# Kernel optimization log

Hardware: AMD Instinct MI355X
Metric: run time of the kernel (lower is better)

## Reference

```python
import jax, jax.numpy as jnp
import numpy as np
import itertools


def exclude_mask(n, d):
    # Boolean mask over d object axes of size n: True iff all indices pairwise distinct.
    if d <= 1:
        return jnp.ones((n,) * d, dtype=bool)
    idx = [jnp.arange(n).reshape((1,) * i + (n,) + (1,) * (d - 1 - i)) for i in range(d)]
    m = jnp.ones((n,) * d, dtype=bool)
    for i in range(d):
        for j in range(i + 1, d):
            m = m & (idx[i] != idx[j])
    return m


def reduce_group(x, d, exclude_self=True):
    # x: [B, n^d (d object axes), C] -> [B, n^(d-1), 2C]
    # exists = max over last object axis (masked to 0), forall = min (masked to 1),
    # interleaved per channel as in torch.stack(..., dim=-1).view(..., 2C).
    if exclude_self and d > 1:
        n = x.shape[1]
        m = exclude_mask(n, d)[None, ..., None]
        x0 = jnp.where(m, x, 0.0)
        x1 = jnp.where(m, x, 1.0)
    else:
        x0 = x1 = x
    ex = jnp.max(x0, axis=-2)
    fa = jnp.min(x1, axis=-2)
    out = jnp.stack([ex, fa], axis=-1)  # [..., C, 2]
    return out.reshape(out.shape[:-2] + (out.shape[-2] * 2,))


def expand_group(x, n):
    # Insert a new object axis of size n just before the channel axis (broadcast).
    return jnp.broadcast_to(jnp.expand_dims(x, -2), x.shape[:-1] + (n, x.shape[-1]))


def permute_group(x, d):
    # Concatenate all d! permutations of the last d object axes along channels.
    if d <= 1:
        return x
    nd = x.ndim
    obj_axes = list(range(nd - 1 - d, nd - 1))
    res = []
    for perm in itertools.permutations(obj_axes):
        p = list(range(0, nd - 1 - d)) + list(perm) + [nd - 1]
        res.append(jnp.transpose(x, p))
    return jnp.concatenate(res, axis=-1)


def mlp(x, W1, b1, W2, b2):
    # InferenceLayer: Linear -> ReLU -> Linear -> Sigmoid, applied on channel dim.
    h = jax.nn.relu(x @ W1 + b1)
    return jax.nn.sigmoid(h @ W2 + b2)


def setup_inputs() -> dict:
    key = jax.random.key(0)
    ks = jax.random.split(key, 24)
    B, n, C, H = 4, 48, 16, 64
    cin = {0: 48, 1: 64, 2: 128, 3: 192}
    inp = {
        "x0": jax.random.uniform(ks[0], (B, C), dtype=jnp.float32),
        "x1": jax.random.uniform(ks[1], (B, n, C), dtype=jnp.float32),
        "x2": jax.random.uniform(ks[2], (B, n, n, C), dtype=jnp.float32),
        "x3": jax.random.uniform(ks[3], (B, n, n, n, C), dtype=jnp.float32),
    }
    for g in range(4):
        inp[f"W1_{g}"] = 0.05 * jax.random.normal(ks[4 + 4 * g], (cin[g], H), dtype=jnp.float32)
        inp[f"b1_{g}"] = jnp.zeros((H,), dtype=jnp.float32)
        inp[f"W2_{g}"] = 0.05 * jax.random.normal(ks[5 + 4 * g], (H, C), dtype=jnp.float32)
        inp[f"b2_{g}"] = jnp.zeros((C,), dtype=jnp.float32)
    return inp


def reference(x0, x1, x2, x3,
              W1_0, b1_0, W2_0, b2_0,
              W1_1, b1_1, W2_1, b2_1,
              W1_2, b1_2, W2_2, b2_2,
              W1_3, b1_3, W2_3, b2_3):
    n = x1.shape[1]
    # group 0: [self, reduce(group1)] -> MLP
    t0 = jnp.concatenate([x0, reduce_group(x1, 1)], axis=-1)            # [B, 48]
    o0 = mlp(t0, W1_0, b1_0, W2_0, b2_0)
    # group 1: [expand(group0), self, reduce(group2)] -> MLP (permuter d=1 is identity)
    t1 = jnp.concatenate([expand_group(x0, n), x1, reduce_group(x2, 2)], axis=-1)  # [B,n,64]
    o1 = mlp(t1, W1_1, b1_1, W2_1, b2_1)
    # group 2: [expand(group1), self, reduce(group3)] -> permute(d=2) -> MLP
    t2 = jnp.concatenate([expand_group(x1, n), x2, reduce_group(x3, 3)], axis=-1)  # [B,n,n,64]
    t2 = permute_group(t2, 2)                                           # [B,n,n,128]
    o2 = mlp(t2, W1_2, b1_2, W2_2, b2_2)
    # group 3: [expand(group2), self] -> permute(d=3) -> MLP
    t3 = jnp.concatenate([expand_group(x2, n), x3], axis=-1)            # [B,n,n,n,32]
    t3 = permute_group(t3, 3)                                           # [B,n,n,n,192]
    o3 = mlp(t3, W1_3, b1_3, W2_3, b2_3)
    return (o0, o1, o2, o3)
```

## Files before the change

### kernel.cpp

```cpp
#include <hip/hip_runtime.h>
#include <math.h>

#define NN 48

typedef __attribute__((ext_vector_type(8))) short bf16x8;
typedef __attribute__((ext_vector_type(4))) float f32x4;

__device__ __forceinline__ float sigmoidf_(float x) {
    return 1.0f / (1.0f + __expf(-x));
}

__device__ __forceinline__ unsigned short f2bf(float f) {
    unsigned u = __float_as_uint(f);
    return (unsigned short)((u + 0x7fffu + ((u >> 16) & 1u)) >> 16);
}

__device__ __forceinline__ unsigned packbf2(float a, float b) {
    return (unsigned)f2bf(a) | ((unsigned)f2bf(b) << 16);
}

__global__ __launch_bounds__(256) void k_pre(const float* __restrict__ x2, const float* __restrict__ x3,
        const float* __restrict__ W1, const float* __restrict__ W2,
        float* __restrict__ r3, unsigned short* __restrict__ wf,
        unsigned short* __restrict__ x2bf, unsigned short* __restrict__ x3bf, int emit) {
    int tid = threadIdx.x, blk = blockIdx.x;
    if (blk < 2304) {
        int posl = tid >> 6, l = tid & 63;
        int pos = blk * 4 + posl;
        int j = pos % NN, i = (pos / NN) % NN;
        int cq = l & 3, kkb = l >> 2;
        float4 ex = make_float4(0.f, 0.f, 0.f, 0.f);
        float4 fa = make_float4(1.f, 1.f, 1.f, 1.f);
        #pragma unroll
        for (int s = 0; s < 3; ++s) {
            int kk = kkb + s * 16;
            size_t idx = (((size_t)pos * NN + kk) << 4) + (cq << 2);
            float4 v = *(const float4*)(x3 + idx);
            if (emit) {
                uint2 pk;
                pk.x = packbf2(v.x, v.y);
                pk.y = packbf2(v.z, v.w);
                *(uint2*)(x3bf + idx) = pk;
            }
            bool ok = (i != j) && (kk != i) && (kk != j);
            ex.x = fmaxf(ex.x, ok ? v.x : 0.f);  fa.x = fminf(fa.x, ok ? v.x : 1.f);
            ex.y = fmaxf(ex.y, ok ? v.y : 0.f);  fa.y = fminf(fa.y, ok ? v.y : 1.f);
            ex.z = fmaxf(ex.z, ok ? v.z : 0.f);  fa.z = fminf(fa.z, ok ? v.z : 1.f);
            ex.w = fmaxf(ex.w, ok ? v.w : 0.f);  fa.w = fminf(fa.w, ok ? v.w : 1.f);
        }
        #pragma unroll
        for (int m = 4; m <= 32; m <<= 1) {
            ex.x = fmaxf(ex.x, __shfl_xor(ex.x, m));  fa.x = fminf(fa.x, __shfl_xor(fa.x, m));
            ex.y = fmaxf(ex.y, __shfl_xor(ex.y, m));  fa.y = fminf(fa.y, __shfl_xor(fa.y, m));
            ex.z = fmaxf(ex.z, __shfl_xor(ex.z, m));  fa.z = fminf(fa.z, __shfl_xor(fa.z, m));
            ex.w = fmaxf(ex.w, __shfl_xor(ex.w, m));  fa.w = fminf(fa.w, __shfl_xor(fa.w, m));
        }
        if (kkb == 0) {
            float* dst = r3 + ((size_t)pos << 5) + (cq << 3);
            *(float4*)dst       = make_float4(ex.x, fa.x, ex.y, fa.y);
            *(float4*)(dst + 4) = make_float4(ex.z, fa.z, ex.w, fa.w);
        }
    } else if (blk < 2340) {
        if (!emit) return;
        int bb = blk - 2304;
        #pragma unroll
        for (int q = 0; q < 4; ++q) {
            int e = bb * 1024 + q * 256 + tid;
            int off = e << 2;
            float4 v = *(const float4*)(x2 + off);
            uint2 pk;
            pk.x = packbf2(v.x, v.y);
            pk.y = packbf2(v.z, v.w);
            *(uint2*)(x2bf + off) = pk;
        }
    } else {
        for (int e = tid; e < 13312; e += 256) {
            unsigned short v;
            if (e < 12288) {
                int idx = e & 7, l = (e >> 3) & 63, r = e >> 9;
                int ks = r % 6, nt = r / 6;
                v = f2bf(W1[(ks * 32 + ((l >> 4) << 3) + idx) * 64 + (nt << 4) + (l & 15)]);
            } else {
                int e2 = e - 12288;
                int idx = e2 & 7, l = (e2 >> 3) & 63, ks = e2 >> 9;
                v = f2bf(W2[(ks * 32 + ((l >> 4) << 3) + idx) * 16 + (l & 15)]);
            }
            wf[e] = v;
        }
    }
}

__global__ __launch_bounds__(256) void k_small(const float* __restrict__ x0, const float* __restrict__ x1,
        const float* __restrict__ x2, const float* __restrict__ r3,
        const float* __restrict__ W1_0, const float* __restrict__ b1_0,
        const float* __restrict__ W2_0, const float* __restrict__ b2_0,
        const float* __restrict__ W1_1, const float* __restrict__ b1_1,
        const float* __restrict__ W2_1, const float* __restrict__ b2_1,
        const float* __restrict__ W1_2, const float* __restrict__ b1_2,
        const float* __restrict__ W2_2, const float* __restrict__ b2_2,
        float* __restrict__ out) {
    __shared__ __align__(16) float smem[8960];
    int tid = threadIdx.x;
    int blk = blockIdx.x;
    if (blk == 0) {
        float* st0 = smem;
        float* sh0 = smem + 192;
        int b = tid >> 6, sub = (tid >> 4) & 3, c = tid & 15;
        float ex = -INFINITY, fa = INFINITY;
        for (int ii = sub * 12; ii < sub * 12 + 12; ++ii) {
            float v = x1[(b * NN + ii) * 16 + c];
            ex = fmaxf(ex, v); fa = fminf(fa, v);
        }
        ex = fmaxf(ex, __shfl_xor(ex, 16)); fa = fminf(fa, __shfl_xor(fa, 16));
        ex = fmaxf(ex, __shfl_xor(ex, 32)); fa = fminf(fa, __shfl_xor(fa, 32));
        if (sub == 0) { st0[b * 48 + 16 + 2 * c] = ex; st0[b * 48 + 17 + 2 * c] = fa; }
        if (tid < 64) st0[(tid >> 4) * 48 + (tid & 15)] = x0[tid];
        __syncthreads();
        {
            int bb = tid >> 6, ln = tid & 63;
            float h = b1_0[ln];
            for (int cc = 0; cc < 48; ++cc) h += st0[bb * 48 + cc] * W1_0[cc * 64 + ln];
            sh0[bb * 64 + ln] = fmaxf(h, 0.f);
        }
        __syncthreads();
        if (tid < 64) {
            int bb = tid >> 4, o = tid & 15;
            float acc = b2_0[o];
            for (int tt = 0; tt < 64; ++tt) acc += sh0[bb * 64 + tt] * W2_0[tt * 16 + o];
            out[bb * 16 + o] = sigmoidf_(acc);
        }
    } else if (blk <= 48) {
        int grp = tid >> 6, ln = tid & 63;
        int row = (blk - 1) * 4 + grp;
        int b = row / NN, i = row % NN;
        float* sin1 = smem + grp * 64;
        float* sh1  = smem + 256 + grp * 64;
        int c = ln & 15, q = ln >> 4;
        float ex = 0.f, fa = 1.f;
        const float* xb = x2 + (size_t)row * NN * 16 + c;
        for (int jj = q * 12; jj < q * 12 + 12; ++jj) {
            float v = xb[jj * 16];
            bool ok = (jj != i);
            ex = fmaxf(ex, ok ? v : 0.f); fa = fminf(fa, ok ? v : 1.f);
        }
        ex = fmaxf(ex, __shfl_xor(ex, 16)); fa = fminf(fa, __shfl_xor(fa, 16));
        ex = fmaxf(ex, __shfl_xor(ex, 32)); fa = fminf(fa, __shfl_xor(fa, 32));
        if (q == 0) { sin1[32 + 2 * c] = ex; sin1[33 + 2 * c] = fa; }
        if (ln < 16) sin1[ln] = x0[b * 16 + ln];
        else if (ln < 32) sin1[ln] = x1[row * 16 + (ln - 16)];
        __syncthreads();
        float h = b1_1[ln];
        #pragma unroll
        for (int c4 = 0; c4 < 64; c4 += 4) {
            float4 iv = *(const float4*)&sin1[c4];
            h += iv.x * W1_1[(c4 + 0) * 64 + ln] + iv.y * W1_1[(c4 + 1) * 64 + ln]
               + iv.z * W1_1[(c4 + 2) * 64 + ln] + iv.w * W1_1[(c4 + 3) * 64 + ln];
        }
        sh1[ln] = fmaxf(h, 0.f);
        __syncthreads();
        if (ln < 16) {
            float acc = b2_1[ln];
            #pragma unroll
            for (int tt = 0; tt < 64; ++tt) acc += sh1[tt] * W2_1[tt * 16 + ln];
            out[64 + row * 16 + ln] = sigmoidf_(acc);
        }
    } else {
        float* sW1  = smem;
        float* sin_ = smem + 8192;
        float* sh   = smem + 8704;
        int wv = tid >> 6, ln = tid & 63;
        for (int p = tid; p < 8192; p += 256) sW1[p] = W1_2[p];
        float bias = b1_2[ln];
        __syncthreads();
        for (int rr = 0; rr < 4; ++rr) {
            int row = (blk - 49) * 16 + rr * 4 + wv;
            int j = row % NN;
            int bi = row / NN;
            int i = bi % NN;
            int b = bi / NN;
            for (int cc = ln; cc < 128; cc += 64) {
                int half = cc >> 6, w = cc & 63;
                int a1 = half ? j : i;
                int a2 = half ? i : j;
                float v;
                if (w < 16)      v = x1[(b * NN + a1) * 16 + w];
                else if (w < 32) v = x2[((b * NN + a1) * NN + a2) * 16 + (w - 16)];
                else             v = r3[((size_t)(b * NN + a1) * NN + a2) * 32 + (w - 32)];
                sin_[wv * 128 + cc] = v;
            }
            __syncthreads();
            float h = bias;
            #pragma unroll
            for (int c4 = 0; c4 < 128; c4 += 4) {
                float4 iv = *(const float4*)&sin_[wv * 128 + c4];
                h += iv.x * sW1[(c4 + 0) * 64 + ln] + iv.y * sW1[(c4 + 1) * 64 + ln]
                   + iv.z * sW1[(c4 + 2) * 64 + ln] + iv.w * sW1[(c4 + 3) * 64 + ln];
            }
            sh[wv * 64 + ln] = fmaxf(h, 0.f);
            __syncthreads();
            if (ln < 16) {
                float acc = b2_2[ln];
                #pragma unroll
                for (int tt = 0; tt < 64; ++tt) acc += sh[wv * 64 + tt] * W2_2[tt * 16 + ln];
                out[3136 + row * 16 + ln] = sigmoidf_(acc);
            }
            __syncthreads();
        }
    }
}

__global__ __launch_bounds__(192) void k_g3d(const unsigned short* __restrict__ x2bf,
        const unsigned short* __restrict__ x3bf, const unsigned short* __restrict__ wf,
        const float* __restrict__ b1, const float* __restrict__ b2,
        float* __restrict__ out3) {
    __shared__ __align__(16) unsigned short sH[2][6 * 64 * 8];

    int tid = threadIdx.x, mt = tid >> 6, l = tid & 63;
    int pp = blockIdx.x, i = 0;
    while (pp >= NN - i) { pp -= NN - i; ++i; }
    int j = i + pp;
    int b = blockIdx.y;

    bf16x8 w1f[4][6];
    #pragma unroll
    for (int nt = 0; nt < 4; ++nt)
        #pragma unroll
        for (int ks = 0; ks < 6; ++ks)
            w1f[nt][ks] = *(const bf16x8*)(wf + (((nt * 6 + ks) << 6) + l) * 8);
    bf16x8 w2f[2];
    #pragma unroll
    for (int ks = 0; ks < 2; ++ks)
        w2f[ks] = *(const bf16x8*)(wf + 12288 + ((ks << 6) + l) * 8);

    const int b2b = b * 36864;
    const int b3b = b * 1769472;
    const int cb2_[6] = { b2b + (i * NN + j) * 16, b2b + i * 768, b2b + (j * NN + i) * 16,
                          b2b + i * 16,            b2b + j * 768, b2b + j * 16 };
    const int cb3_[6] = { b3b + (i * NN + j) * 768, b3b + i * 36864 + j * 16, b3b + (j * NN + i) * 768,
                          b3b + i * 768 + j * 16,   b3b + j * 36864 + i * 16, b3b + j * 768 + i * 16 };
    const int s2_[6] = { 0, 16, 0, 768, 16, 768 };
    const int s3_[6] = { 16, 768, 16, 36864, 768, 36864 };

    int l15 = l & 15, g = l >> 4;
    bool isx2 = (g < 2);
    int goff = (g & 1) << 3;
    const unsigned short* bp = isx2 ? x2bf : x3bf;
    int off_[6];
    #pragma unroll
    for (int f = 0; f < 6; ++f) {
        int s = isx2 ? s2_[f] : s3_[f];
        int base = isx2 ? cb2_[f] : cb3_[f];
        off_[f] = base + ((mt << 4) + l15) * s + goff;
    }

    f32x4 acc[4][2];
    #pragma unroll
    for (int nt = 0; nt < 4; ++nt) {
        float bv = b1[(nt << 4) + l15];
        f32x4 t = {bv, bv, bv, bv};
        acc[nt][0] = t; acc[nt][1] = t;
    }
    const int p1[6] = { 2, 4, 0, 5, 1, 3 };

    #pragma unroll
    for (int f = 0; f < 6; ++f) {
        bf16x8 a = *(const bf16x8*)(bp + off_[f]);
        #pragma unroll
        for (int nt = 0; nt < 4; ++nt) {
            acc[nt][0] = __builtin_amdgcn_mfma_f32_16x16x32_bf16(a, w1f[nt][f], acc[nt][0], 0, 0, 0);
            acc[nt][1] = __builtin_amdgcn_mfma_f32_16x16x32_bf16(a, w1f[nt][p1[f]], acc[nt][1], 0, 0, 0);
        }
    }

    {
        int rbase = (l >> 4) << 2;
        #pragma unroll
        for (int tr = 0; tr < 2; ++tr) {
            #pragma unroll
            for (int nt = 0; nt < 4; ++nt) {
                int within = ((nt & 1) << 4) + l15;
                int ks2 = nt >> 1;
                int lhi = (within >> 3) << 4;
                int idx = within & 7;
                #pragma unroll
                for (int rg = 0; rg < 4; ++rg) {
                    float h = fmaxf(acc[nt][tr][rg], 0.0f);
                    int lp = rbase + rg + lhi;
                    sH[tr][((((mt << 1) + ks2) << 6) + lp) * 8 + idx] = f2bf(h);
                }
            }
        }
    }
    __syncthreads();

    {
        float bv2 = b2[l15];
        #pragma unroll
        for (int tr = 0; tr < 2; ++tr) {
            if (tr == 0 || i != j) {
                f32x4 acc2 = {bv2, bv2, bv2, bv2};
                #pragma unroll
                for (int ks = 0; ks < 2; ++ks) {
                    bf16x8 a = *(const bf16x8*)&sH[tr][((((mt << 1) + ks) << 6) + l) << 3];
                    acc2 = __builtin_amdgcn_mfma_f32_16x16x32_bf16(a, w2f[ks], acc2, 0, 0, 0);
                }
                int triple = tr ? ((b * NN + j) * NN + i) : ((b * NN + i) * NN + j);
                size_t obase = ((size_t)triple * NN + (mt << 4) + ((l >> 4) << 2)) * 16 + l15;
                #pragma unroll
                for (int rg = 0; rg < 4; ++rg)
                    out3[obase + (size_t)rg * 16] = sigmoidf_(acc2[rg]);
            }
        }
    }
}

__global__ __launch_bounds__(256) void k_g3m(const float* __restrict__ x2, const float* __restrict__ x3,
                                             const unsigned short* __restrict__ wf,
                                             const float* __restrict__ b1, const float* __restrict__ b2,
                                             float* __restrict__ out3) {
    __shared__ __align__(16) unsigned short sA[18 * 64 * 8];
    __shared__ __align__(16) unsigned short sH[6 * 64 * 8];

    int tid = threadIdx.x;
    int wv = tid >> 6, l = tid & 63;
    int triple = blockIdx.x;
    int j = triple % NN;
    int bi = triple / NN;
    int i = bi % NN;
    int b = bi / NN;

    bf16x8 w1f[6];
    #pragma unroll
    for (int ks = 0; ks < 6; ++ks)
        w1f[ks] = *(const bf16x8*)(wf + (((wv * 6 + ks) << 6) + l) * 8);
    bf16x8 w2f[2];
    #pragma unroll
    for (int ks = 0; ks < 2; ++ks)
        w2f[ks] = *(const bf16x8*)(wf + 12288 + ((ks << 6) + l) * 8);

    const int x2b = b * NN * NN * 16;
    const int x3b = b * NN * NN * NN * 16;

    #pragma unroll
    for (int it = 0; it < 9; ++it) {
        int t = it * 256 + tid;
        int fs = __builtin_amdgcn_readfirstlane(t >> 7);
        int mt = fs / 6;
        int ks = fs - mt * 6;
        int lp = (t >> 1) & 63;
        int kk = (mt << 4) + (lp & 15);
        int w = ((lp >> 4) << 3) + ((t & 1) << 2);
        int a1, a2, a3;
        switch (ks) {
            case 0:  a1 = i;  a2 = j;  a3 = kk; break;
            case 1:  a1 = i;  a2 = kk; a3 = j;  break;
            case 2:  a1 = j;  a2 = i;  a3 = kk; break;
            case 3:  a1 = kk; a2 = i;  a3 = j;  break;
            case 4:  a1 = j;  a2 = kk; a3 = i;  break;
            default: a1 = kk; a2 = j;  a3 = i;  break;
        }
        const float* p2 = x2 + x2b + (a1 * NN + a2) * 16 + w;
        const float* p3 = x3 + x3b + ((a1 * NN + a2) * NN + a3) * 16 + (w - 16);
        const float* p = (w < 16) ? p2 : p3;
        float4 v = *(const float4*)p;
        uint2 pk;
        pk.x = packbf2(v.x, v.y);
        pk.y = packbf2(v.z, v.w);
        *(uint2*)&sA[t * 4] = pk;
    }
    __syncthreads();

    float bv = b1[(wv << 4) + (l & 15)];
    f32x4 acc0 = {bv, bv, bv, bv};
    f32x4 acc1 = acc0, acc2 = acc0;
    #pragma unroll
    for (int ks = 0; ks < 6; ++ks) {
        bf16x8 a0  = *(const bf16x8*)&sA[(((0 * 6 + ks) << 6) + l) << 3];
        bf16x8 a1_ = *(const bf16x8*)&sA[(((1 * 6 + ks) << 6) + l) << 3];
        bf16x8 a2_ = *(const bf16x8*)&sA[(((2 * 6 + ks) << 6) + l) << 3];
        acc0 = __builtin_amdgcn_mfma_f32_16x16x32_bf16(a0,  w1f[ks], acc0, 0, 0, 0);
        acc1 = __builtin_amdgcn_mfma_f32_16x16x32_bf16(a1_, w1f[ks], acc1, 0, 0, 0);
        acc2 = __builtin_amdgcn_mfma_f32_16x16x32_bf16(a2_, w1f[ks], acc2, 0, 0, 0);
    }

    {
        int within = ((wv & 1) << 4) + (l & 15);
        int ks2 = wv >> 1;
        int lhi = (within >> 3) << 4;
        int idx = within & 7;
        int rbase = (l >> 4) << 2;
        #pragma unroll
        for (int mt = 0; mt < 3; ++mt) {
            f32x4 a = (mt == 0) ? acc0 : (mt == 1) ? acc1 : acc2;
            #pragma unroll
            for (int rg = 0; rg < 4; ++rg) {
                float h = fmaxf(a[rg], 0.0f);
                int lp = rbase + rg + lhi;
                sH[((((mt << 1) + ks2) << 6) + lp) * 8 + idx] = f2bf(h);
            }
        }
    }
    __syncthreads();

    if (wv < 3) {
        int mt = wv;
        float bv2 = b2[l & 15];
        f32x4 acc = {bv2, bv2, bv2, bv2};
        #pragma unroll
        for (int ks = 0; ks < 2; ++ks) {
            bf16x8 a = *(const bf16x8*)&sH[((((mt << 1) + ks) << 6) + l) << 3];
            acc = __builtin_amdgcn_mfma_f32_16x16x32_bf16(a, w2f[ks], acc, 0, 0, 0);
        }
        size_t obase = ((size_t)triple * NN + (mt << 4) + ((l >> 4) << 2)) * 16 + (l & 15);
        #pragma unroll
        for (int rg = 0; rg < 4; ++rg)
            out3[obase + (size_t)rg * 16] = sigmoidf_(acc[rg]);
    }
}

extern "C" void kernel_launch(void* const* d_in, const int* in_sizes, int n_in,
                              void* d_out, int out_size, void* d_ws, size_t ws_size,
                              hipStream_t stream) {
    const float* x0 = (const float*)d_in[0];
    const float* x1 = (const float*)d_in[1];
    const float* x2 = (const float*)d_in[2];
    const float* x3 = (const float*)d_in[3];
    const float* W1_0 = (const float*)d_in[4];
    const float* b1_0 = (const float*)d_in[5];
    const float* W2_0 = (const float*)d_in[6];
    const float* b2_0 = (const float*)d_in[7];
    const float* W1_1 = (const float*)d_in[8];
    const float* b1_1 = (const float*)d_in[9];
    const float* W2_1 = (const float*)d_in[10];
    const float* b2_1 = (const float*)d_in[11];
    const float* W1_2 = (const float*)d_in[12];
    const float* b1_2 = (const float*)d_in[13];
    const float* W2_2 = (const float*)d_in[14];
    const float* b2_2 = (const float*)d_in[15];
    const float* W1_3 = (const float*)d_in[16];
    const float* b1_3 = (const float*)d_in[17];
    const float* W2_3 = (const float*)d_in[18];
    const float* b2_3 = (const float*)d_in[19];

    float* out = (float*)d_out;
    float* r3 = (float*)d_ws;
    unsigned short* wf   = (unsigned short*)(r3 + 294912);
    unsigned short* x2bf = wf + 13312;
    unsigned short* x3bf = x2bf + 147456;
    size_t need = (size_t)294912 * 4 + (size_t)(13312 + 147456 + 7077888) * 2;
    int fast = (ws_size >= need) ? 1 : 0;

    hipLaunchKernelGGL(k_pre, dim3(2341), dim3(256), 0, stream,
                       x2, x3, W1_3, W2_3, r3, wf, x2bf, x3bf, fast);
    if (fast)
        hipLaunchKernelGGL(k_g3d, dim3(1176, 4), dim3(192), 0, stream,
                           x2bf, x3bf, wf, b1_3, b2_3, out + 150592);
    else
        hipLaunchKernelGGL(k_g3m, dim3(9216), dim3(256), 0, stream,
                           x2, x3, wf, b1_3, b2_3, out + 150592);
    hipLaunchKernelGGL(k_small, dim3(625), dim3(256), 0, stream,
                       x0, x1, x2, r3,
                       W1_0, b1_0, W2_0, b2_0,
                       W1_1, b1_1, W2_1, b2_1,
                       W1_2, b1_2, W2_2, b2_2,
                       out);
}
```

Before: 81.00 us.

## Stage layer-3 W1 weights in LDS and process four pairs per block

The group-3 MFMA kernel now copies the packed bf16 weights into shared memory once per block instead of holding all 24 W1 fragments in registers. Each block loops over four (i,j) pairs, so the weight load is paid once for four pairs. The first-layer MFMA loop is regrouped to pair permutation slices so each weight fragment read from LDS is used twice. The barrier between the hidden write and the second matmul is dropped, since each wave reads only its own hidden rows. Fewer registers should allow higher occupancy, at the cost of extra LDS traffic per MFMA and four times fewer blocks.

```diff
diff --git a/kernel.cpp b/kernel.cpp
--- a/kernel.cpp
+++ b/kernel.cpp
@@ -213,102 +213,115 @@
         const unsigned short* __restrict__ x3bf, const unsigned short* __restrict__ wf,
         const float* __restrict__ b1, const float* __restrict__ b2,
         float* __restrict__ out3) {
+    __shared__ __align__(16) unsigned short sW[13312];
     __shared__ __align__(16) unsigned short sH[2][6 * 64 * 8];
 
     int tid = threadIdx.x, mt = tid >> 6, l = tid & 63;
-    int pp = blockIdx.x, i = 0;
-    while (pp >= NN - i) { pp -= NN - i; ++i; }
-    int j = i + pp;
     int b = blockIdx.y;
 
-    bf16x8 w1f[4][6];
-    #pragma unroll
-    for (int nt = 0; nt < 4; ++nt)
-        #pragma unroll
-        for (int ks = 0; ks < 6; ++ks)
-            w1f[nt][ks] = *(const bf16x8*)(wf + (((nt * 6 + ks) << 6) + l) * 8);
-    bf16x8 w2f[2];
-    #pragma unroll
-    for (int ks = 0; ks < 2; ++ks)
-        w2f[ks] = *(const bf16x8*)(wf + 12288 + ((ks << 6) + l) * 8);
-
-    const int b2b = b * 36864;
-    const int b3b = b * 1769472;
-    const int cb2_[6] = { b2b + (i * NN + j) * 16, b2b + i * 768, b2b + (j * NN + i) * 16,
-                          b2b + i * 16,            b2b + j * 768, b2b + j * 16 };
-    const int cb3_[6] = { b3b + (i * NN + j) * 768, b3b + i * 36864 + j * 16, b3b + (j * NN + i) * 768,
-                          b3b + i * 768 + j * 16,   b3b + j * 36864 + i * 16, b3b + j * 768 + i * 16 };
-    const int s2_[6] = { 0, 16, 0, 768, 16, 768 };
-    const int s3_[6] = { 16, 768, 16, 36864, 768, 36864 };
+    for (int t = tid; t < 3328; t += 192)
+        *(uint2*)&sW[t * 4] = *(const uint2*)(wf + t * 4);
+    __syncthreads();
 
     int l15 = l & 15, g = l >> 4;
     bool isx2 = (g < 2);
     int goff = (g & 1) << 3;
     const unsigned short* bp = isx2 ? x2bf : x3bf;
-    int off_[6];
-    #pragma unroll
-    for (int f = 0; f < 6; ++f) {
-        int s = isx2 ? s2_[f] : s3_[f];
-        int base = isx2 ? cb2_[f] : cb3_[f];
-        off_[f] = base + ((mt << 4) + l15) * s + goff;
-    }
-
-    f32x4 acc[4][2];
-    #pragma unroll
-    for (int nt = 0; nt < 4; ++nt) {
-        float bv = b1[(nt << 4) + l15];
-        f32x4 t = {bv, bv, bv, bv};
-        acc[nt][0] = t; acc[nt][1] = t;
-    }
-    const int p1[6] = { 2, 4, 0, 5, 1, 3 };
-
-    #pragma unroll
-    for (int f = 0; f < 6; ++f) {
-        bf16x8 a = *(const bf16x8*)(bp + off_[f]);
+
+    float b1v[4];
+    #pragma unroll
+    for (int nt = 0; nt < 4; ++nt) b1v[nt] = b1[(nt << 4) + l15];
+    float b2v = b2[l15];
+
+    bf16x8 w2f[2];
+    #pragma unroll
+    for (int ks = 0; ks < 2; ++ks)
+        w2f[ks] = *(const bf16x8*)&sW[12288 + ((ks << 6) + l) * 8];
+
+    const int b2b = b * 36864;
+    const int b3b = b * 1769472;
+    const int s2_[6] = { 0, 16, 0, 768, 16, 768 };
+    const int s3_[6] = { 16, 768, 16, 36864, 768, 36864 };
+    const int fpa[3] = { 0, 1, 3 };
+    const int fpb[3] = { 2, 4, 5 };
+
+    #pragma unroll 1
+    for (int pr = 0; pr < 4; ++pr) {
+        int pp = blockIdx.x * 4 + pr, i = 0;
+        while (pp >= NN - i) { pp -= NN - i; ++i; }
+        int j = i + pp;
+
+        const int cb2_[6] = { b2b + (i * NN + j) * 16, b2b + i * 768, b2b + (j * NN + i) * 16,
+                              b2b + i * 16,            b2b + j * 768, b2b + j * 16 };
+        const int cb3_[6] = { b3b + (i * NN + j) * 768, b3b + i * 36864 + j * 16, b3b + (j * NN + i) * 768,
+                              b3b + i * 768 + j * 16,   b3b + j * 36864 + i * 16, b3b + j * 768 + i * 16 };
+        int off_[6];
+        #pragma unroll
+        for (int f = 0; f < 6; ++f) {
+            int s = isx2 ? s2_[f] : s3_[f];
+            int base = isx2 ? cb2_[f] : cb3_[f];
+            off_[f] = base + ((mt << 4) + l15) * s + goff;
+        }
+
+        f32x4 acc[4][2];
         #pragma unroll
         for (int nt = 0; nt < 4; ++nt) {
-            acc[nt][0] = __builtin_amdgcn_mfma_f32_16x16x32_bf16(a, w1f[nt][f], acc[nt][0], 0, 0, 0);
-            acc[nt][1] = __builtin_amdgcn_mfma_f32_16x16x32_bf16(a, w1f[nt][p1[f]], acc[nt][1], 0, 0, 0);
-        }
-    }
-
-    {
-        int rbase = (l >> 4) << 2;
-        #pragma unroll
-        for (int tr = 0; tr < 2; ++tr) {
+            f32x4 t = {b1v[nt], b1v[nt], b1v[nt], b1v[nt]};
+            acc[nt][0] = t; acc[nt][1] = t;
+        }
+
+        #pragma unroll
+        for (int fp = 0; fp < 3; ++fp) {
+            int fa = fpa[fp], fb = fpb[fp];
+            bf16x8 aA = *(const bf16x8*)(bp + off_[fa]);
+            bf16x8 aB = *(const bf16x8*)(bp + off_[fb]);
             #pragma unroll
             for (int nt = 0; nt < 4; ++nt) {
-                int within = ((nt & 1) << 4) + l15;
-                int ks2 = nt >> 1;
-                int lhi = (within >> 3) << 4;
-                int idx = within & 7;
+                bf16x8 wA = *(const bf16x8*)&sW[(((nt * 6 + fa) << 6) + l) * 8];
+                bf16x8 wB = *(const bf16x8*)&sW[(((nt * 6 + fb) << 6) + l) * 8];
+                acc[nt][0] = __builtin_amdgcn_mfma_f32_16x16x32_bf16(aA, wA, acc[nt][0], 0, 0, 0);
+                acc[nt][1] = __builtin_amdgcn_mfma_f32_16x16x32_bf16(aA, wB, acc[nt][1], 0, 0, 0);
+                acc[nt][0] = __builtin_amdgcn_mfma_f32_16x16x32_bf16(aB, wB, acc[nt][0], 0, 0, 0);
+                acc[nt][1] = __builtin_amdgcn_mfma_f32_16x16x32_bf16(aB, wA, acc[nt][1], 0, 0, 0);
+            }
+        }
+
+        {
+            int rbase = (l >> 4) << 2;
+            #pragma unroll
+            for (int tr = 0; tr < 2; ++tr) {
                 #pragma unroll
-                for (int rg = 0; rg < 4; ++rg) {
-                    float h = fmaxf(acc[nt][tr][rg], 0.0f);
-                    int lp = rbase + rg + lhi;
-                    sH[tr][((((mt << 1) + ks2) << 6) + lp) * 8 + idx] = f2bf(h);
+                for (int nt = 0; nt < 4; ++nt) {
+                    int within = ((nt & 1) << 4) + l15;
+                    int ks2 = nt >> 1;
+                    int lhi = (within >> 3) << 4;
+                    int idx = within & 7;
+                    #pragma unroll
+                    for (int rg = 0; rg < 4; ++rg) {
+                        float h = fmaxf(acc[nt][tr][rg], 0.0f);
+                        int lp = rbase + rg + lhi;
+                        sH[tr][((((mt << 1) + ks2) << 6) + lp) * 8 + idx] = f2bf(h);
+                    }
                 }
             }
         }
-    }
-    __syncthreads();
-
-    {
-        float bv2 = b2[l15];
-        #pragma unroll
-        for (int tr = 0; tr < 2; ++tr) {
-            if (tr == 0 || i != j) {
-                f32x4 acc2 = {bv2, bv2, bv2, bv2};
-                #pragma unroll
-                for (int ks = 0; ks < 2; ++ks) {
-                    bf16x8 a = *(const bf16x8*)&sH[tr][((((mt << 1) + ks) << 6) + l) << 3];
-                    acc2 = __builtin_amdgcn_mfma_f32_16x16x32_bf16(a, w2f[ks], acc2, 0, 0, 0);
+
+        {
+            #pragma unroll
+            for (int tr = 0; tr < 2; ++tr) {
+                if (tr == 0 || i != j) {
+                    f32x4 acc2 = {b2v, b2v, b2v, b2v};
+                    #pragma unroll
+                    for (int ks = 0; ks < 2; ++ks) {
+                        bf16x8 a = *(const bf16x8*)&sH[tr][((((mt << 1) + ks) << 6) + l) << 3];
+                        acc2 = __builtin_amdgcn_mfma_f32_16x16x32_bf16(a, w2f[ks], acc2, 0, 0, 0);
+                    }
+                    int triple = tr ? ((b * NN + j) * NN + i) : ((b * NN + i) * NN + j);
+                    size_t obase = ((size_t)triple * NN + (mt << 4) + ((l >> 4) << 2)) * 16 + l15;
+                    #pragma unroll
+                    for (int rg = 0; rg < 4; ++rg)
+                        out3[obase + (size_t)rg * 16] = sigmoidf_(acc2[rg]);
                 }
-                int triple = tr ? ((b * NN + j) * NN + i) : ((b * NN + i) * NN + j);
-                size_t obase = ((size_t)triple * NN + (mt << 4) + ((l >> 4) << 2)) * 16 + l15;
-                #pragma unroll
-                for (int rg = 0; rg < 4; ++rg)
-                    out3[obase + (size_t)rg * 16] = sigmoidf_(acc2[rg]);
             }
         }
     }
@@ -453,7 +466,7 @@
     hipLaunchKernelGGL(k_pre, dim3(2341), dim3(256), 0, stream,
                        x2, x3, W1_3, W2_3, r3, wf, x2bf, x3bf, fast);
     if (fast)
-        hipLaunchKernelGGL(k_g3d, dim3(1176, 4), dim3(192), 0, stream,
+        hipLaunchKernelGGL(k_g3d, dim3(294, 4), dim3(192), 0, stream,
                            x2bf, x3bf, wf, b1_3, b2_3, out + 150592);
     else
         hipLaunchKernelGGL(k_g3m, dim3(9216), dim3(256), 0, stream,
```

Result: slower. 96.42 us (+19.0%).

## Stage group-3 input tiles in LDS and split waves over hidden columns

Applied to the files above, without the earlier changes.

The group-3 kernel now uses 256 threads. Each block first copies its bf16 x2/x3 input fragments for all six permutations into shared memory, using coalesced 8-byte loads. Each wave then owns one 16-column slice of the hidden layer instead of one row tile, so each wave keeps only 6 W1 fragments in registers rather than 24. This is meant to cut register pressure, raise occupancy and replace strided direct global loads. The cost is an extra LDS round trip, a barrier, and a second GEMM that only three of the four waves run.

```diff
diff --git a/kernel.cpp b/kernel.cpp
--- a/kernel.cpp
+++ b/kernel.cpp
@@ -209,82 +209,92 @@
     }
 }
 
-__global__ __launch_bounds__(192) void k_g3d(const unsigned short* __restrict__ x2bf,
+__global__ __launch_bounds__(256) void k_g3p(const unsigned short* __restrict__ x2bf,
         const unsigned short* __restrict__ x3bf, const unsigned short* __restrict__ wf,
         const float* __restrict__ b1, const float* __restrict__ b2,
         float* __restrict__ out3) {
+    __shared__ __align__(16) unsigned short sA[18 * 64 * 8];
     __shared__ __align__(16) unsigned short sH[2][6 * 64 * 8];
 
-    int tid = threadIdx.x, mt = tid >> 6, l = tid & 63;
+    int tid = threadIdx.x;
+    int wv = tid >> 6, l = tid & 63;
     int pp = blockIdx.x, i = 0;
     while (pp >= NN - i) { pp -= NN - i; ++i; }
     int j = i + pp;
     int b = blockIdx.y;
 
-    bf16x8 w1f[4][6];
-    #pragma unroll
-    for (int nt = 0; nt < 4; ++nt)
-        #pragma unroll
-        for (int ks = 0; ks < 6; ++ks)
-            w1f[nt][ks] = *(const bf16x8*)(wf + (((nt * 6 + ks) << 6) + l) * 8);
+    bf16x8 w1f[6];
+    #pragma unroll
+    for (int ks = 0; ks < 6; ++ks)
+        w1f[ks] = *(const bf16x8*)(wf + (((wv * 6 + ks) << 6) + l) * 8);
     bf16x8 w2f[2];
     #pragma unroll
     for (int ks = 0; ks < 2; ++ks)
         w2f[ks] = *(const bf16x8*)(wf + 12288 + ((ks << 6) + l) * 8);
 
-    const int b2b = b * 36864;
-    const int b3b = b * 1769472;
-    const int cb2_[6] = { b2b + (i * NN + j) * 16, b2b + i * 768, b2b + (j * NN + i) * 16,
-                          b2b + i * 16,            b2b + j * 768, b2b + j * 16 };
-    const int cb3_[6] = { b3b + (i * NN + j) * 768, b3b + i * 36864 + j * 16, b3b + (j * NN + i) * 768,
-                          b3b + i * 768 + j * 16,   b3b + j * 36864 + i * 16, b3b + j * 768 + i * 16 };
-    const int s2_[6] = { 0, 16, 0, 768, 16, 768 };
-    const int s3_[6] = { 16, 768, 16, 36864, 768, 36864 };
-
-    int l15 = l & 15, g = l >> 4;
-    bool isx2 = (g < 2);
-    int goff = (g & 1) << 3;
-    const unsigned short* bp = isx2 ? x2bf : x3bf;
-    int off_[6];
-    #pragma unroll
-    for (int f = 0; f < 6; ++f) {
-        int s = isx2 ? s2_[f] : s3_[f];
-        int base = isx2 ? cb2_[f] : cb3_[f];
-        off_[f] = base + ((mt << 4) + l15) * s + goff;
-    }
-
-    f32x4 acc[4][2];
-    #pragma unroll
-    for (int nt = 0; nt < 4; ++nt) {
-        float bv = b1[(nt << 4) + l15];
+    const int x2b = b * 36864;
+    const int x3b = b * 1769472;
+
+    #pragma unroll
+    for (int it = 0; it < 9; ++it) {
+        int t = it * 256 + tid;
+        int fs = __builtin_amdgcn_readfirstlane(t >> 7);
+        int mt = fs / 6;
+        int ks = fs - mt * 6;
+        int lp = (t >> 1) & 63;
+        int kk = (mt << 4) + (lp & 15);
+        int w = ((lp >> 4) << 3) + ((t & 1) << 2);
+        int a1, a2, a3;
+        switch (ks) {
+            case 0:  a1 = i;  a2 = j;  a3 = kk; break;
+            case 1:  a1 = i;  a2 = kk; a3 = j;  break;
+            case 2:  a1 = j;  a2 = i;  a3 = kk; break;
+            case 3:  a1 = kk; a2 = i;  a3 = j;  break;
+            case 4:  a1 = j;  a2 = kk; a3 = i;  break;
+            default: a1 = kk; a2 = j;  a3 = i;  break;
+        }
+        const unsigned short* p2 = x2bf + x2b + (a1 * NN + a2) * 16 + w;
+        const unsigned short* p3 = x3bf + x3b + ((a1 * NN + a2) * NN + a3) * 16 + (w - 16);
+        const unsigned short* p = (w < 16) ? p2 : p3;
+        *(uint2*)&sA[t * 4] = *(const uint2*)p;
+    }
+    __syncthreads();
+
+    float bv = b1[(wv << 4) + (l & 15)];
+    f32x4 acc0[3], acc1[3];
+    #pragma unroll
+    for (int mt = 0; mt < 3; ++mt) {
         f32x4 t = {bv, bv, bv, bv};
-        acc[nt][0] = t; acc[nt][1] = t;
-    }
-    const int p1[6] = { 2, 4, 0, 5, 1, 3 };
-
-    #pragma unroll
-    for (int f = 0; f < 6; ++f) {
-        bf16x8 a = *(const bf16x8*)(bp + off_[f]);
-        #pragma unroll
-        for (int nt = 0; nt < 4; ++nt) {
-            acc[nt][0] = __builtin_amdgcn_mfma_f32_16x16x32_bf16(a, w1f[nt][f], acc[nt][0], 0, 0, 0);
-            acc[nt][1] = __builtin_amdgcn_mfma_f32_16x16x32_bf16(a, w1f[nt][p1[f]], acc[nt][1], 0, 0, 0);
-        }
+        acc0[mt] = t; acc1[mt] = t;
+    }
+    const int p1q[6] = { 2, 4, 0, 5, 1, 3 };
+    #pragma unroll
+    for (int ks = 0; ks < 6; ++ks) {
+        bf16x8 a0 = *(const bf16x8*)&sA[(((0 * 6 + ks) << 6) + l) << 3];
+        bf16x8 a1_ = *(const bf16x8*)&sA[(((1 * 6 + ks) << 6) + l) << 3];
+        bf16x8 a2_ = *(const bf16x8*)&sA[(((2 * 6 + ks) << 6) + l) << 3];
+        acc0[0] = __builtin_amdgcn_mfma_f32_16x16x32_bf16(a0,  w1f[ks],      acc0[0], 0, 0, 0);
+        acc1[0] = __builtin_amdgcn_mfma_f32_16x16x32_bf16(a0,  w1f[p1q[ks]], acc1[0], 0, 0, 0);
+        acc0[1] = __builtin_amdgcn_mfma_f32_16x16x32_bf16(a1_, w1f[ks],      acc0[1], 0, 0, 0);
+        acc1[1] = __builtin_amdgcn_mfma_f32_16x16x32_bf16(a1_, w1f[p1q[ks]], acc1[1], 0, 0, 0);
+        acc0[2] = __builtin_amdgcn_mfma_f32_16x16x32_bf16(a2_, w1f[ks],      acc0[2], 0, 0, 0);
+        acc1[2] = __builtin_amdgcn_mfma_f32_16x16x32_bf16(a2_, w1f[p1q[ks]], acc1[2], 0, 0, 0);
     }
 
     {
+        int within = ((wv & 1) << 4) + (l & 15);
+        int ks2 = wv >> 1;
+        int lhi = (within >> 3) << 4;
+        int idx = within & 7;
         int rbase = (l >> 4) << 2;
         #pragma unroll
         for (int tr = 0; tr < 2; ++tr) {
             #pragma unroll
-            for (int nt = 0; nt < 4; ++nt) {
-                int within = ((nt & 1) << 4) + l15;
-                int ks2 = nt >> 1;
-                int lhi = (within >> 3) << 4;
-                int idx = within & 7;
+            for (int mt = 0; mt < 3; ++mt) {
+                f32x4 a = tr ? acc1[mt] : acc0[mt];
                 #pragma unroll
                 for (int rg = 0; rg < 4; ++rg) {
-                    float h = fmaxf(acc[nt][tr][rg], 0.0f);
+                    float h = fmaxf(a[rg], 0.0f);
                     int lp = rbase + rg + lhi;
                     sH[tr][((((mt << 1) + ks2) << 6) + lp) * 8 + idx] = f2bf(h);
                 }
@@ -293,8 +303,9 @@
     }
     __syncthreads();
 
-    {
-        float bv2 = b2[l15];
+    if (wv < 3) {
+        int mt = wv;
+        float bv2 = b2[l & 15];
         #pragma unroll
         for (int tr = 0; tr < 2; ++tr) {
             if (tr == 0 || i != j) {
@@ -305,7 +316,7 @@
                     acc2 = __builtin_amdgcn_mfma_f32_16x16x32_bf16(a, w2f[ks], acc2, 0, 0, 0);
                 }
                 int triple = tr ? ((b * NN + j) * NN + i) : ((b * NN + i) * NN + j);
-                size_t obase = ((size_t)triple * NN + (mt << 4) + ((l >> 4) << 2)) * 16 + l15;
+                size_t obase = ((size_t)triple * NN + (mt << 4) + ((l >> 4) << 2)) * 16 + (l & 15);
                 #pragma unroll
                 for (int rg = 0; rg < 4; ++rg)
                     out3[obase + (size_t)rg * 16] = sigmoidf_(acc2[rg]);
@@ -453,7 +464,7 @@
     hipLaunchKernelGGL(k_pre, dim3(2341), dim3(256), 0, stream,
                        x2, x3, W1_3, W2_3, r3, wf, x2bf, x3bf, fast);
     if (fast)
-        hipLaunchKernelGGL(k_g3d, dim3(1176, 4), dim3(192), 0, stream,
+        hipLaunchKernelGGL(k_g3p, dim3(1176, 4), dim3(256), 0, stream,
                            x2bf, x3bf, wf, b1_3, b2_3, out + 150592);
     else
         hipLaunchKernelGGL(k_g3m, dim3(9216), dim3(256), 0, stream,
```

New measurement: 85.36 us. +5.4%, slower.
